# Performance work log

Measured on AMD Instinct MI355X. Metric: run time of the kernel, lower is better.

## Reference

```python
import jax, jax.numpy as jnp
import numpy as np


def setup_inputs() -> dict:
    key = jax.random.key(0)
    kA, kB = jax.random.split(key)
    B, H, W, C = 8, 48, 48, 256
    feature_A = jax.random.normal(kA, (B, H, W, C), dtype=jnp.float32)
    feature_B = jax.random.normal(kB, (B, H, W, C), dtype=jnp.float32)
    return {"feature_A": feature_A, "feature_B": feature_B}


def reference(feature_A, feature_B):
    # corr[b,i,j,k,l] = mean_c A[b,i,j,c] * B[b,k,l,c]
    # Expressed as a batched GEMM over the channel dim instead of the
    # naive [B,H,W,H,W,C] broadcast intermediate.
    C = feature_A.shape[-1]
    corr = jnp.einsum('bijc,bklc->bijkl', feature_A, feature_B) / C
    # L2 norm over source positions (i,j) per target position (k,l)
    penalty = jnp.sqrt(jnp.sum(corr * corr, axis=(1, 2), keepdims=True))  # [B,1,1,H,W]
    return corr / penalty
```

## Files before the change

### kernel.cpp

```cpp
#include <hip/hip_runtime.h>


#define HW2 2304
#define CH  256
#define NB  8
#define NELEM (NB * HW2 * CH)

typedef __attribute__((ext_vector_type(8))) short bf16x8;
typedef __attribute__((ext_vector_type(4))) float f32x4;

static __device__ inline unsigned short f2bf(float f) {
    union { float f; unsigned u; } x; x.f = f;
    unsigned r = x.u + 0x7FFFu + ((x.u >> 16) & 1u);
    return (unsigned short)(r >> 16);
}

static __device__ inline float bf2f(unsigned short u) {
    union { unsigned u; float f; } x; x.u = ((unsigned)u) << 16;
    return x.f;
}

static __device__ inline void async_copy16(const void* g, void* l) {
    __builtin_amdgcn_global_load_lds(
        (const __attribute__((address_space(1))) unsigned int*)g,
        (__attribute__((address_space(3))) unsigned int*)l, 16, 0, 0);
}

__global__ __launch_bounds__(256) void convert_bf16(const float* __restrict__ A,
                                                    const float* __restrict__ B,
                                                    unsigned short* __restrict__ Abf,
                                                    unsigned short* __restrict__ Bbf,
                                                    unsigned short* __restrict__ Atbf) {
    __shared__ unsigned short t[64][65];
    const int blk = blockIdx.x;
    const bool isA = blk < 1152;
    const int tb = isA ? blk : blk - 1152;
    const int b  = tb / 144;
    const int tt = tb % 144;
    const int ijt = tt >> 2, ct = tt & 3;
    const size_t base = ((size_t)b * HW2 + (size_t)ijt * 64) * CH + ct * 64;
    const float* src = (isA ? A : B) + base;
    unsigned short* dst = (isA ? Abf : Bbf) + base;
    const int tid = threadIdx.x;
    const int lr = tid & 15, rq = tid >> 4;
#pragma unroll
    for (int p = 0; p < 4; p++) {
        const int row = rq + p * 16;
        float4 v = *(const float4*)(src + (size_t)row * CH + lr * 4);
        ushort4 u;
        u.x = f2bf(v.x); u.y = f2bf(v.y); u.z = f2bf(v.z); u.w = f2bf(v.w);
        *(ushort4*)(dst + (size_t)row * CH + lr * 4) = u;
        if (isA) {
            t[row][lr * 4 + 0] = u.x; t[row][lr * 4 + 1] = u.y;
            t[row][lr * 4 + 2] = u.z; t[row][lr * 4 + 3] = u.w;
        }
    }
    if (isA) {
        __syncthreads();
#pragma unroll
        for (int p = 0; p < 4; p++) {
            const int c = rq + p * 16;
            ushort4 u;
            u.x = t[lr * 4 + 0][c]; u.y = t[lr * 4 + 1][c];
            u.z = t[lr * 4 + 2][c]; u.w = t[lr * 4 + 3][c];
            *(ushort4*)(Atbf + ((size_t)b * CH + (size_t)(ct * 64 + c)) * HW2
                        + (size_t)ijt * 64 + lr * 4) = u;
        }
    }
}

__global__ __launch_bounds__(256) void gram(const unsigned short* __restrict__ Atbf,
                                            unsigned short* __restrict__ Gbf) {
    __shared__ unsigned short As[2][4096];
    __shared__ unsigned short Bs[2][4096];
    const int tid = threadIdx.x;
    const int bx = blockIdx.x, by = blockIdx.y, b = blockIdx.z;
    const unsigned short* Ar = Atbf + ((size_t)b * CH + by * 64) * HW2;
    const unsigned short* Br = Atbf + ((size_t)b * CH + bx * 64) * HW2;
    const int srow = tid >> 2, skcol = (tid & 3) * 8;
    const int wave = tid >> 6, lane = tid & 63;
    const int wm = (wave >> 1) * 32, wn = (wave & 1) * 32;
    const int lr = lane & 15, quad = lane >> 4, k8 = quad * 8;

    f32x4 acc[2][2];
#pragma unroll
    for (int i = 0; i < 2; i++)
#pragma unroll
        for (int j = 0; j < 2; j++) acc[i][j] = (f32x4){0.f, 0.f, 0.f, 0.f};

#define G_STAGE(bufi, kt)                                                      \
    {                                                                          \
        _Pragma("unroll")                                                      \
        for (int c2 = 0; c2 < 2; c2++) {                                       \
            async_copy16(Ar + (size_t)srow * HW2 + (kt) + c2 * 32 + skcol,     \
                         &As[bufi][c2 * 2048 + tid * 8]);                      \
            async_copy16(Br + (size_t)srow * HW2 + (kt) + c2 * 32 + skcol,     \
                         &Bs[bufi][c2 * 2048 + tid * 8]);                      \
        }                                                                      \
    }

    G_STAGE(0, 0);
    __syncthreads();
    for (int t = 0; t < 36; t++) {
        const int buf = t & 1;
        if (t < 35) G_STAGE(buf ^ 1, (t + 1) * 64);
#pragma unroll
        for (int c2 = 0; c2 < 2; c2++) {
            bf16x8 af[2], bfr[2];
#pragma unroll
            for (int mt = 0; mt < 2; mt++)
                af[mt] = *(const bf16x8*)&As[buf][c2 * 2048 + (wm + mt * 16 + lr) * 32 + k8];
#pragma unroll
            for (int nt = 0; nt < 2; nt++)
                bfr[nt] = *(const bf16x8*)&Bs[buf][c2 * 2048 + (wn + nt * 16 + lr) * 32 + k8];
#pragma unroll
            for (int mt = 0; mt < 2; mt++)
#pragma unroll
                for (int nt = 0; nt < 2; nt++)
                    acc[mt][nt] = __builtin_amdgcn_mfma_f32_16x16x32_bf16(
                        af[mt], bfr[nt], acc[mt][nt], 0, 0, 0);
        }
        __syncthreads();
    }
#pragma unroll
    for (int mt = 0; mt < 2; mt++)
#pragma unroll
        for (int nt = 0; nt < 2; nt++) {
            const int row = by * 64 + wm + mt * 16 + quad * 4;
            const int col = bx * 64 + wn + nt * 16 + lr;
#pragma unroll
            for (int r = 0; r < 4; r++)
                Gbf[((size_t)b * CH + row + r) * CH + col] = f2bf(acc[mt][nt][r]);
        }
}

__global__ __launch_bounds__(256) void colsq(const unsigned short* __restrict__ Bbf,
                                             const unsigned short* __restrict__ Gbf,
                                             float* __restrict__ cs0,
                                             float* __restrict__ cs1) {
    __shared__ unsigned short As[2][4096];
    __shared__ unsigned short Bs[2][8192];
    __shared__ float colSqL[64];
    const int tid = threadIdx.x;
    const int bx = blockIdx.x;
    const int by = blockIdx.y;
    const int b  = blockIdx.z;
    const unsigned short* Ab = Bbf + ((size_t)b * HW2 + by * 64) * CH;
    const unsigned short* Gb = Gbf + ((size_t)b * CH + bx * 128) * CH;
    const int srow = tid >> 2, skcol = (tid & 3) * 8;
    const int wave = tid >> 6, lane = tid & 63;
    const int wm = (wave >> 1) * 32, wn = (wave & 1) * 64;
    const int lr = lane & 15, quad = lane >> 4, k8 = quad * 8;

    f32x4 acc[2][4];
#pragma unroll
    for (int i = 0; i < 2; i++)
#pragma unroll
        for (int j = 0; j < 4; j++) acc[i][j] = (f32x4){0.f, 0.f, 0.f, 0.f};

#define C_STAGE(bufi, kt)                                                      \
    {                                                                          \
        _Pragma("unroll")                                                      \
        for (int c2 = 0; c2 < 2; c2++) {                                       \
            async_copy16(Ab + (size_t)srow * CH + (kt) + c2 * 32 + skcol,      \
                         &As[bufi][c2 * 2048 + tid * 8]);                      \
            _Pragma("unroll")                                                  \
            for (int i = 0; i < 2; i++)                                        \
                async_copy16(Gb + (size_t)(srow + i * 64) * CH + (kt) + c2 * 32 + skcol, \
                             &Bs[bufi][c2 * 4096 + tid * 8 + i * 2048]);       \
        }                                                                      \
    }

    C_STAGE(0, 0);
    __syncthreads();
    for (int t = 0; t < 4; t++) {
        const int buf = t & 1;
        if (t < 3) C_STAGE(buf ^ 1, (t + 1) * 64);
#pragma unroll
        for (int c2 = 0; c2 < 2; c2++) {
            bf16x8 af[2], bfr[4];
#pragma unroll
            for (int mt = 0; mt < 2; mt++)
                af[mt] = *(const bf16x8*)&As[buf][c2 * 2048 + (wm + mt * 16 + lr) * 32 + k8];
#pragma unroll
            for (int nt = 0; nt < 4; nt++)
                bfr[nt] = *(const bf16x8*)&Bs[buf][c2 * 4096 + (wn + nt * 16 + lr) * 32 + k8];
#pragma unroll
            for (int mt = 0; mt < 2; mt++)
#pragma unroll
                for (int nt = 0; nt < 4; nt++)
                    acc[mt][nt] = __builtin_amdgcn_mfma_f32_16x16x32_bf16(
                        af[mt], bfr[nt], acc[mt][nt], 0, 0, 0);
        }
        __syncthreads();
    }

    if (tid < 64) colSqL[tid] = 0.f;
    __syncthreads();
#pragma unroll
    for (int mt = 0; mt < 2; mt++)
#pragma unroll
        for (int r = 0; r < 4; r++) {
            const int lrow = wm + mt * 16 + quad * 4 + r;
            float s = 0.f;
#pragma unroll
            for (int nt = 0; nt < 4; nt++) {
                const int col = bx * 128 + wn + nt * 16 + lr;
                s += acc[mt][nt][r] * bf2f(Ab[(size_t)lrow * CH + col]);
            }
            s += __shfl_xor(s, 1); s += __shfl_xor(s, 2);
            s += __shfl_xor(s, 4); s += __shfl_xor(s, 8);
            if (lr == 0) atomicAdd(&colSqL[lrow], s);
        }
    __syncthreads();
    if (tid < 64)
        (bx == 0 ? cs0 : cs1)[(size_t)b * HW2 + by * 64 + tid] = colSqL[tid];
}

__global__ __launch_bounds__(256) void corr_out(const unsigned short* __restrict__ Abf,
                                                const unsigned short* __restrict__ Bbf,
                                                const float* __restrict__ cs0,
                                                const float* __restrict__ cs1,
                                                float* __restrict__ out) {
    __shared__ unsigned short As[2 * 128 * 32];
    __shared__ unsigned short Bs[2 * 128 * 32];

    const int tid = threadIdx.x;

    const int lin = blockIdx.x + 18 * (blockIdx.y + 18 * blockIdx.z);
    const int b  = lin & 7;
    const int r_ = lin >> 3;
    const int bx = r_ % 18;
    const int by = r_ / 18;

    const unsigned short* Ab = Abf + ((size_t)b * HW2 + (size_t)by * 128) * CH;
    const unsigned short* Bb = Bbf + ((size_t)b * HW2 + (size_t)bx * 128) * CH;

    const int srow  = tid >> 2;
    const int skcol = (tid & 3) * 8;

    const int wave = tid >> 6;
    const int lane = tid & 63;
    const int wm   = (wave >> 1) * 64;
    const int wn   = (wave & 1) * 64;
    const int lr   = lane & 15;
    const int quad = lane >> 4;
    const int k8   = quad * 8;

    f32x4 acc[4][4];
#pragma unroll
    for (int i = 0; i < 4; i++)
#pragma unroll
        for (int j = 0; j < 4; j++) acc[i][j] = (f32x4){0.f, 0.f, 0.f, 0.f};

    for (int kt = 0; kt < CH; kt += 64) {
#pragma unroll
        for (int c = 0; c < 2; c++) {
            const int kof = kt + c * 32;
#pragma unroll
            for (int i = 0; i < 2; i++) {
                async_copy16(Ab + (size_t)(srow + i * 64) * CH + kof + skcol,
                             &As[c * 4096 + tid * 8 + i * 2048]);
                async_copy16(Bb + (size_t)(srow + i * 64) * CH + kof + skcol,
                             &Bs[c * 4096 + tid * 8 + i * 2048]);
            }
        }
        __syncthreads();
#pragma unroll
        for (int c = 0; c < 2; c++) {
            bf16x8 af[4], bfr[4];
#pragma unroll
            for (int mt = 0; mt < 4; mt++)
                af[mt] = *(const bf16x8*)&As[c * 4096 + (wm + mt * 16 + lr) * 32 + k8];
#pragma unroll
            for (int nt = 0; nt < 4; nt++)
                bfr[nt] = *(const bf16x8*)&Bs[c * 4096 + (wn + nt * 16 + lr) * 32 + k8];
#pragma unroll
            for (int mt = 0; mt < 4; mt++)
#pragma unroll
                for (int nt = 0; nt < 4; nt++)
                    acc[mt][nt] = __builtin_amdgcn_mfma_f32_16x16x32_bf16(
                        af[mt], bfr[nt], acc[mt][nt], 0, 0, 0);
        }
        __syncthreads();
    }

    const int colBase = bx * 128 + wn;
    const size_t outBase = (size_t)b * HW2 * HW2;
    const float* c0 = cs0 + (size_t)b * HW2;
    const float* c1 = cs1 + (size_t)b * HW2;
#pragma unroll
    for (int nt = 0; nt < 4; nt++) {
        const int col = colBase + nt * 16 + lr;
        const float rinv = rsqrtf(c0[col] + c1[col]);
#pragma unroll
        for (int mt = 0; mt < 4; mt++) {
            const int row0 = by * 128 + wm + mt * 16 + quad * 4;
            f32x4 v = acc[mt][nt];
#pragma unroll
            for (int r = 0; r < 4; r++)
                out[outBase + (size_t)(row0 + r) * HW2 + col] = v[r] * rinv;
        }
    }
}

extern "C" void kernel_launch(void* const* d_in, const int* in_sizes, int n_in,
                              void* d_out, int out_size, void* d_ws, size_t ws_size,
                              hipStream_t stream) {
    const float* A = (const float*)d_in[0];
    const float* B = (const float*)d_in[1];
    float* out = (float*)d_out;

    unsigned short* Abf  = (unsigned short*)d_ws;
    unsigned short* Bbf  = Abf + NELEM;
    unsigned short* Atbf = Bbf + NELEM;
    unsigned short* Gbf  = Atbf + NELEM;
    float* cs0 = (float*)(Gbf + (size_t)NB * CH * CH);
    float* cs1 = cs0 + (size_t)NB * HW2;

    convert_bf16<<<2304, 256, 0, stream>>>(A, B, Abf, Bbf, Atbf);
    gram<<<dim3(4, 4, NB), 256, 0, stream>>>(Atbf, Gbf);
    colsq<<<dim3(2, 36, NB), 256, 0, stream>>>(Bbf, Gbf, cs0, cs1);
    corr_out<<<dim3(18, 18, NB), 256, 0, stream>>>(Abf, Bbf, cs0, cs1, out);
}
```

Before: 250.1 us.

## Split-K the Gram kernel and stage output tile through LDS for coalesced stores

The Gram-matrix GEMM is split along its long reduction dimension into six partial blocks, and a new reduction kernel sums the fp32 partials and converts them to bf16. This raises the grid from 128 to 768 blocks so the GPU is better filled. The final correlation kernel now writes its accumulator tile into shared memory and then stores each row as a float4, with the normalisation applied per column, instead of scattering scalar stores. The cost is extra partial-buffer traffic, one more kernel launch, and additional LDS barriers in the epilogue.

```diff
diff --git a/kernel.cpp b/kernel.cpp
--- a/kernel.cpp
+++ b/kernel.cpp
@@ -5,6 +5,7 @@
 #define CH  256
 #define NB  8
 #define NELEM (NB * HW2 * CH)
+#define KSG 6
 
 typedef __attribute__((ext_vector_type(8))) short bf16x8;
 typedef __attribute__((ext_vector_type(4))) float f32x4;
@@ -69,12 +70,14 @@
     }
 }
 
-__global__ __launch_bounds__(256) void gram(const unsigned short* __restrict__ Atbf,
-                                            unsigned short* __restrict__ Gbf) {
+__global__ __launch_bounds__(256) void gram_part(const unsigned short* __restrict__ Atbf,
+                                                 float* __restrict__ Gp) {
     __shared__ unsigned short As[2][4096];
     __shared__ unsigned short Bs[2][4096];
     const int tid = threadIdx.x;
-    const int bx = blockIdx.x, by = blockIdx.y, b = blockIdx.z;
+    const int bx = blockIdx.x, by = blockIdx.y;
+    const int b  = blockIdx.z / KSG, ks = blockIdx.z % KSG;
+    const int kt0 = ks * (HW2 / KSG);
     const unsigned short* Ar = Atbf + ((size_t)b * CH + by * 64) * HW2;
     const unsigned short* Br = Atbf + ((size_t)b * CH + bx * 64) * HW2;
     const int srow = tid >> 2, skcol = (tid & 3) * 8;
@@ -99,11 +102,11 @@
         }                                                                      \
     }
 
-    G_STAGE(0, 0);
+    G_STAGE(0, kt0);
     __syncthreads();
-    for (int t = 0; t < 36; t++) {
+    for (int t = 0; t < 6; t++) {
         const int buf = t & 1;
-        if (t < 35) G_STAGE(buf ^ 1, (t + 1) * 64);
+        if (t < 5) G_STAGE(buf ^ 1, kt0 + (t + 1) * 64);
 #pragma unroll
         for (int c2 = 0; c2 < 2; c2++) {
             bf16x8 af[2], bfr[2];
@@ -122,6 +125,7 @@
         }
         __syncthreads();
     }
+    float* Gpb = Gp + ((size_t)(ks * NB + b)) * (CH * CH);
 #pragma unroll
     for (int mt = 0; mt < 2; mt++)
 #pragma unroll
@@ -130,8 +134,22 @@
             const int col = bx * 64 + wn + nt * 16 + lr;
 #pragma unroll
             for (int r = 0; r < 4; r++)
-                Gbf[((size_t)b * CH + row + r) * CH + col] = f2bf(acc[mt][nt][r]);
-        }
+                Gpb[(size_t)(row + r) * CH + col] = acc[mt][nt][r];
+        }
+}
+
+__global__ __launch_bounds__(256) void g2bf_sum(const float* __restrict__ Gp,
+                                                unsigned short* __restrict__ Gbf) {
+    const int f = blockIdx.x * 256 + threadIdx.x;
+    float4 s = {0.f, 0.f, 0.f, 0.f};
+#pragma unroll
+    for (int ks = 0; ks < KSG; ks++) {
+        float4 v = ((const float4*)(Gp + (size_t)ks * NB * CH * CH))[f];
+        s.x += v.x; s.y += v.y; s.z += v.z; s.w += v.w;
+    }
+    ushort4 u;
+    u.x = f2bf(s.x); u.y = f2bf(s.y); u.z = f2bf(s.z); u.w = f2bf(s.w);
+    ((ushort4*)Gbf)[f] = u;
 }
 
 __global__ __launch_bounds__(256) void colsq(const unsigned short* __restrict__ Bbf,
@@ -217,13 +235,14 @@
         (bx == 0 ? cs0 : cs1)[(size_t)b * HW2 + by * 64 + tid] = colSqL[tid];
 }
 
-__global__ __launch_bounds__(256) void corr_out(const unsigned short* __restrict__ Abf,
-                                                const unsigned short* __restrict__ Bbf,
-                                                const float* __restrict__ cs0,
-                                                const float* __restrict__ cs1,
-                                                float* __restrict__ out) {
-    __shared__ unsigned short As[2 * 128 * 32];
-    __shared__ unsigned short Bs[2 * 128 * 32];
+__global__ __launch_bounds__(256) void corr_norm(const unsigned short* __restrict__ Abf,
+                                                 const unsigned short* __restrict__ Bbf,
+                                                 const float* __restrict__ cs0,
+                                                 const float* __restrict__ cs1,
+                                                 float* __restrict__ out) {
+    __shared__ __align__(16) unsigned char smem[64 * 132 * 4];
+    unsigned short* As = (unsigned short*)smem;
+    unsigned short* Bs = As + 8192;
 
     const int tid = threadIdx.x;
 
@@ -238,14 +257,9 @@
 
     const int srow  = tid >> 2;
     const int skcol = (tid & 3) * 8;
-
-    const int wave = tid >> 6;
-    const int lane = tid & 63;
-    const int wm   = (wave >> 1) * 64;
-    const int wn   = (wave & 1) * 64;
-    const int lr   = lane & 15;
-    const int quad = lane >> 4;
-    const int k8   = quad * 8;
+    const int wave = tid >> 6, lane = tid & 63;
+    const int wm = (wave >> 1) * 64, wn = (wave & 1) * 64;
+    const int lr = lane & 15, quad = lane >> 4, k8 = quad * 8;
 
     f32x4 acc[4][4];
 #pragma unroll
@@ -285,22 +299,42 @@
         __syncthreads();
     }
 
-    const int colBase = bx * 128 + wn;
+    const int c4 = tid & 31;
+    const int colG0 = bx * 128 + c4 * 4;
+    float4 s0 = *(const float4*)(cs0 + (size_t)b * HW2 + colG0);
+    float4 s1 = *(const float4*)(cs1 + (size_t)b * HW2 + colG0);
+    float4 rv;
+    rv.x = rsqrtf(s0.x + s1.x);
+    rv.y = rsqrtf(s0.y + s1.y);
+    rv.z = rsqrtf(s0.z + s1.z);
+    rv.w = rsqrtf(s0.w + s1.w);
+
+    float* T = (float*)smem;
+    const int rbase = tid >> 5;
     const size_t outBase = (size_t)b * HW2 * HW2;
-    const float* c0 = cs0 + (size_t)b * HW2;
-    const float* c1 = cs1 + (size_t)b * HW2;
-#pragma unroll
-    for (int nt = 0; nt < 4; nt++) {
-        const int col = colBase + nt * 16 + lr;
-        const float rinv = rsqrtf(c0[col] + c1[col]);
-#pragma unroll
-        for (int mt = 0; mt < 4; mt++) {
-            const int row0 = by * 128 + wm + mt * 16 + quad * 4;
-            f32x4 v = acc[mt][nt];
-#pragma unroll
-            for (int r = 0; r < 4; r++)
-                out[outBase + (size_t)(row0 + r) * HW2 + col] = v[r] * rinv;
-        }
+
+#pragma unroll
+    for (int p = 0; p < 2; p++) {
+        if ((wave >> 1) == p) {
+#pragma unroll
+            for (int mt = 0; mt < 4; mt++)
+#pragma unroll
+                for (int nt = 0; nt < 4; nt++) {
+                    f32x4 v = acc[mt][nt];
+#pragma unroll
+                    for (int r = 0; r < 4; r++)
+                        T[(mt * 16 + quad * 4 + r) * 132 + wn + nt * 16 + lr] = v[r];
+                }
+        }
+        __syncthreads();
+#pragma unroll
+        for (int k = 0; k < 8; k++) {
+            const int row = rbase + 8 * k;
+            float4 v = *(const float4*)&T[row * 132 + c4 * 4];
+            v.x *= rv.x; v.y *= rv.y; v.z *= rv.z; v.w *= rv.w;
+            *(float4*)&out[outBase + (size_t)(by * 128 + p * 64 + row) * HW2 + colG0] = v;
+        }
+        __syncthreads();
     }
 }
 
@@ -315,11 +349,15 @@
     unsigned short* Bbf  = Abf + NELEM;
     unsigned short* Atbf = Bbf + NELEM;
     unsigned short* Gbf  = Atbf + NELEM;
-    float* cs0 = (float*)(Gbf + (size_t)NB * CH * CH);
+    float* Gp  = (float*)(Gbf + (size_t)NB * CH * CH);
+    float* cs0 = Gp + (size_t)KSG * NB * CH * CH;
     float* cs1 = cs0 + (size_t)NB * HW2;
 
     convert_bf16<<<2304, 256, 0, stream>>>(A, B, Abf, Bbf, Atbf);
-    gram<<<dim3(4, 4, NB), 256, 0, stream>>>(Atbf, Gbf);
+    gram_part<<<dim3(4, 4, NB * KSG), 256, 0, stream>>>(Atbf, Gp);
+    g2bf_sum<<<512, 256, 0, stream>>>(Gp, Gbf);
     colsq<<<dim3(2, 36, NB), 256, 0, stream>>>(Bbf, Gbf, cs0, cs1);
-    corr_out<<<dim3(18, 18, NB), 256, 0, stream>>>(Abf, Bbf, cs0, cs1, out);
-}
+
+    dim3 grid(HW2 / 128, HW2 / 128, NB);
+    corr_norm<<<grid, 256, 0, stream>>>(Abf, Bbf, cs0, cs1, out);
+}
```

After: 240.1 us. 4.0% less time.
